# Performance work log

Measured on AMD Instinct MI355X. Metric: run time of the kernel, lower is better.

## Reference

```python
import jax, jax.numpy as jnp
import numpy as np

B, OBS, LAT, NXT, E, HG, H = 8192, 128, 32, 128, 8, 256, 256


def setup_inputs() -> dict:
    key = jax.random.key(0)
    ks = jax.random.split(key, 20)
    d_in = OBS + LAT

    def w(k, shape, fan_in):
        return jax.random.uniform(k, shape, jnp.float32, -1.0, 1.0) * (np.sqrt(3.0) / np.sqrt(fan_in)).astype(np.float32)

    inp = {
        "x": jax.random.normal(ks[0], (B, OBS), jnp.float32),
        "z": jax.random.normal(ks[1], (B, LAT), jnp.float32),
        # gating MLP: (obs+lat) -> hg -> hg -> hg -> E
        "gw0": w(ks[2], (d_in, HG), d_in), "gb0": jnp.zeros((HG,), jnp.float32),
        "gw1": w(ks[3], (HG, HG), HG),    "gb1": jnp.zeros((HG,), jnp.float32),
        "gw2": w(ks[4], (HG, HG), HG),    "gb2": jnp.zeros((HG,), jnp.float32),
        "gw3": w(ks[5], (HG, E), HG),     "gb3": jnp.zeros((E,), jnp.float32),
        # expert weight stacks (kaiming-uniform-style init, bias = 0.01)
        "w0": w(ks[6], (E, d_in, H), d_in * H),      "b0": jnp.full((E, H), 0.01, jnp.float32),
        "w1": w(ks[7], (E, H + LAT, H), (H + LAT) * H), "b1": jnp.full((E, H), 0.01, jnp.float32),
        "w2": w(ks[8], (E, H + LAT, NXT), (H + LAT) * NXT), "b2": jnp.full((E, NXT), 0.01, jnp.float32),
    }
    return inp


def reference(x, z, gw0, gb0, gw1, gb1, gw2, gb2, gw3, gb3, w0, b0, w1, b1, w2, b2):
    xz = jnp.concatenate((x, z), axis=1)  # [B, obs+lat]
    # gating MLP (ELU activations, linear head) -> softmax coefficients over experts
    g = jax.nn.elu(xz @ gw0 + gb0)
    g = jax.nn.elu(g @ gw1 + gb1)
    g = jax.nn.elu(g @ gw2 + gb2)
    coef = jax.nn.softmax(g @ gw3 + gb3, axis=1)  # [B, E]

    layer_out = x
    for w, b, act in ((w0, b0, jax.nn.elu), (w1, b1, jax.nn.elu), (w2, b2, None)):
        inp = jnp.concatenate((layer_out, z), axis=1)  # [B, i]
        # coefficient-weighted expert mixing fused with the per-sample matvec:
        # equals (coef @ flat_weight).view(B,i,o) consumed by baddbmm in the original
        out = jnp.einsum('bi,eio,be->bo', inp, w, coef) + coef @ b
        layer_out = act(out) if act is not None else out
    return layer_out
```

## Files before the change

### kernel.cpp

```cpp
#include <hip/hip_runtime.h>
#include <hip/hip_bf16.h>

typedef _Float16 half_t;
typedef __attribute__((ext_vector_type(8))) _Float16 half8;
typedef __attribute__((ext_vector_type(4))) _Float16 half4;
typedef __attribute__((ext_vector_type(4))) float float4v;
typedef __attribute__((ext_vector_type(2))) float float2v;

#define BSZ 8192
#define NT 1024
#define ACTSTR 280
#define XSTR 152
#define ZSTR 40

#define OFF_SX 0
#define OFF_SB0 (OFF_SX + 32 * XSTR)
#define OFF_SB1 (OFF_SB0 + 32 * ACTSTR)
#define OFF_SZ (OFF_SB1 + 32 * ACTSTR)
#define HALFS_TOTAL (OFF_SZ + 32 * ZSTR)
#define OFF_LOG_B (HALFS_TOTAL * 2)
#define OFF_CF_B (OFF_LOG_B + 1024)
#define SMEM_BYTES 131072

__device__ __forceinline__ float elu_fast(float v) {
    return v > 0.f ? v : (__expf(v) - 1.f);
}

template <int EXPP, int NPASS, int CH, int MT, bool ZLAST, int ACT, int DST>
__device__ __forceinline__ void layer_run(
    const half_t* sSrc, int sstr, const half_t* sZ,
    const half_t* __restrict__ W, int NS,
    const float* __restrict__ bias, int biasN, const float* sCf,
    half_t* sDst, float* __restrict__ gOut, int ldg,
    int row0, int strip, int mrow, int lane, int l15, int quad) {
    constexpr int TOT = NPASS * CH;
    const size_t estr = (size_t)NS * CH * 512;
    const int col = strip * 16 + l15;
    const half_t* aBase = sSrc + (mrow + l15) * sstr + quad * 8;
    const half_t* zBase = sZ + (mrow + l15) * ZSTR + quad * 8;

    const half_t* wp = W + (size_t)strip * CH * 512 + lane * 8;
    int c_i = 0;
    const float* bp = bias + col;
    int c_c = 0, h_c = 0;

    half8 B0[EXPP], B1[EXPP], A0[MT], A1[MT];
    float part[MT][4];
    float bv[EXPP];
    float4v acc[EXPP][MT];

    auto issue = [&](half8(&B)[EXPP], half8(&A)[MT]) {
#pragma unroll
        for (int e = 0; e < EXPP; ++e) B[e] = *(const half8*)&wp[(size_t)e * estr];
#pragma unroll
        for (int mt = 0; mt < MT; ++mt)
            A[mt] = (ZLAST && c_i == CH - 1)
                        ? *(const half8*)&zBase[mt * 16 * ZSTR]
                        : *(const half8*)&aBase[mt * 16 * sstr + c_i * 32];
        wp += 512;
        if (++c_i == CH) { c_i = 0; wp += (size_t)EXPP * estr - (size_t)CH * 512; }
    };

    auto body = [&](half8(&B)[EXPP], half8(&A)[MT]) {
        if (c_c == 0) {
#pragma unroll
            for (int e = 0; e < EXPP; ++e) bv[e] = bp[(size_t)e * biasN];
#pragma unroll
            for (int e = 0; e < EXPP; ++e)
#pragma unroll
                for (int mt = 0; mt < MT; ++mt) acc[e][mt] = (float4v){0.f, 0.f, 0.f, 0.f};
        }
#pragma unroll
        for (int e = 0; e < EXPP; ++e)
#pragma unroll
            for (int mt = 0; mt < MT; ++mt)
                acc[e][mt] = __builtin_amdgcn_mfma_f32_16x16x32_f16(A[mt], B[e], acc[e][mt], 0, 0, 0);
        if (c_c == CH - 1) {
#pragma unroll
            for (int mt = 0; mt < MT; ++mt)
#pragma unroll
                for (int r = 0; r < 4; ++r) {
                    const int rl = mrow + mt * 16 + quad * 4 + r;
                    float val;
                    if constexpr (EXPP * NPASS == 1) {
                        val = acc[0][mt][r] + bv[0];
                    } else {
                        const float2v cf = *(const float2v*)&sCf[rl * 8 + h_c * EXPP];
                        val = cf[0] * (acc[0][mt][r] + bv[0]);
                        val += cf[1] * (acc[1][mt][r] + bv[1]);
                    }
                    part[mt][r] = (h_c == 0) ? val : part[mt][r] + val;
                    if (h_c == NPASS - 1) {
                        float o = part[mt][r];
                        if (DST == 0) {
                            if (ACT) o = elu_fast(o);
                            sDst[rl * ACTSTR + col] = (half_t)o;
                        } else {
                            gOut[(size_t)(row0 + rl) * ldg + col] = o;
                        }
                    }
                }
            bp += (size_t)EXPP * biasN;
        }
        if (++c_c == CH) { c_c = 0; ++h_c; }
    };

    issue(B0, A0);
    int it = 0;
#pragma unroll 1
    for (; it + 2 < TOT; it += 2) {
        issue(B1, A1);
        body(B0, A0);
        issue(B0, A0);
        body(B1, A1);
    }
    if constexpr (TOT % 2 == 0) {
        issue(B1, A1);
        body(B0, A0);
        body(B1, A1);
    } else {
        body(B0, A0);
    }
}

__device__ __forceinline__ void layer_logits(
    const half_t* sSrc, const half_t* __restrict__ W,
    const float* __restrict__ bias, float* sLog, int wv, int lane, int l15, int quad) {
    if (wv != 0) return;
    float4v acc[2] = {(float4v){0.f, 0.f, 0.f, 0.f}, (float4v){0.f, 0.f, 0.f, 0.f}};
#pragma unroll
    for (int c = 0; c < 8; ++c) {
        half8 a0 = *(const half8*)&sSrc[l15 * ACTSTR + c * 32 + quad * 8];
        half8 a1 = *(const half8*)&sSrc[(16 + l15) * ACTSTR + c * 32 + quad * 8];
        half8 b = *(const half8*)&W[c * 512 + lane * 8];
        acc[0] = __builtin_amdgcn_mfma_f32_16x16x32_f16(a0, b, acc[0], 0, 0, 0);
        acc[1] = __builtin_amdgcn_mfma_f32_16x16x32_f16(a1, b, acc[1], 0, 0, 0);
    }
    if (l15 < 8) {
        const float bvv = bias[l15];
#pragma unroll
        for (int mt = 0; mt < 2; ++mt)
#pragma unroll
            for (int r = 0; r < 4; ++r)
                sLog[(mt * 16 + quad * 4 + r) * 8 + l15] = acc[mt][r] + bvv;
    }
}

__global__ __launch_bounds__(NT) void fused_mann(
    const float* __restrict__ x, const float* __restrict__ z,
    const half_t* __restrict__ Wg0, const half_t* __restrict__ Wg1,
    const half_t* __restrict__ Wg2, const half_t* __restrict__ Wg3,
    const float* __restrict__ gb0, const float* __restrict__ gb1,
    const float* __restrict__ gb2, const float* __restrict__ gb3,
    const half_t* __restrict__ W0, const half_t* __restrict__ W1,
    const half_t* __restrict__ W2, const float* __restrict__ b0,
    const float* __restrict__ b1, const float* __restrict__ b2,
    float* __restrict__ out) {
    extern __shared__ __align__(16) char dynsm[];
    half_t* sm = (half_t*)dynsm;
    half_t* sX = sm + OFF_SX;
    half_t* sB0 = sm + OFF_SB0;
    half_t* sB1 = sm + OFF_SB1;
    half_t* sZ = sm + OFF_SZ;
    float* sLog = (float*)(dynsm + OFF_LOG_B);
    float* sCf = (float*)(dynsm + OFF_CF_B);

    const int tid = threadIdx.x;
    const int row0 = blockIdx.x * 32;
    const int lane = tid & 63, wv = tid >> 6;
    const int l15 = lane & 15, quad = lane >> 4;

    for (int i = tid; i < 32 * 128; i += NT) {
        int r = i >> 7, c = i & 127;
        sX[r * XSTR + c] = (half_t)x[(size_t)(row0 + r) * 128 + c];
    }
    for (int i = tid; i < 32 * 32; i += NT) {
        int r = i >> 5, c = i & 31;
        sZ[r * ZSTR + c] = (half_t)z[(size_t)(row0 + r) * 32 + c];
    }
    __syncthreads();

    layer_run<1, 1, 5, 2, true, 1, 0>(sX, XSTR, sZ, Wg0, 16, gb0, 256, nullptr,
                                      sB0, nullptr, 0, row0, wv, 0, lane, l15, quad);
    __syncthreads();
    layer_run<1, 1, 8, 2, false, 1, 0>(sB0, ACTSTR, sZ, Wg1, 16, gb1, 256, nullptr,
                                       sB1, nullptr, 0, row0, wv, 0, lane, l15, quad);
    __syncthreads();
    layer_run<1, 1, 8, 2, false, 1, 0>(sB1, ACTSTR, sZ, Wg2, 16, gb2, 256, nullptr,
                                       sB0, nullptr, 0, row0, wv, 0, lane, l15, quad);
    __syncthreads();
    layer_logits(sB0, Wg3, gb3, sLog, wv, lane, l15, quad);
    __syncthreads();
    if (tid < 32) {
        float v[8], m = -1e30f;
#pragma unroll
        for (int e = 0; e < 8; ++e) { v[e] = sLog[tid * 8 + e]; m = fmaxf(m, v[e]); }
        float sum = 0.f;
#pragma unroll
        for (int e = 0; e < 8; ++e) { v[e] = __expf(v[e] - m); sum += v[e]; }
        float inv = 1.f / sum;
#pragma unroll
        for (int e = 0; e < 8; ++e) sCf[tid * 8 + e] = v[e] * inv;
    }
    __syncthreads();
    layer_run<2, 4, 5, 2, true, 1, 0>(sX, XSTR, sZ, W0, 16, b0, 256, sCf,
                                      sB1, nullptr, 0, row0, wv, 0, lane, l15, quad);
    __syncthreads();
    layer_run<2, 4, 9, 2, true, 1, 0>(sB1, ACTSTR, sZ, W1, 16, b1, 256, sCf,
                                      sB0, nullptr, 0, row0, wv, 0, lane, l15, quad);
    __syncthreads();
    layer_run<2, 4, 9, 1, true, 0, 2>(sB0, ACTSTR, sZ, W2, 8, b2, 128, sCf,
                                      nullptr, out, 128, row0, wv & 7, (wv >> 3) * 16,
                                      lane, l15, quad);
}

struct WDesc { const float* src; half_t* dst; int K, N, Npad, blk0; };
struct WPack { WDesc d[7]; };

__global__ __launch_bounds__(256) void conv_w_all(WPack pk) {
    __shared__ float t[32][33];
    const int bid = blockIdx.x;
    int di = 0;
#pragma unroll
    for (int i = 1; i < 7; ++i)
        if (bid >= pk.d[i].blk0) di = i;
    const WDesc d = pk.d[di];
    const int NS = d.Npad >> 4, CHN = d.K >> 5;
    const int ntiles = d.Npad / 32, ktiles = CHN;
    int local = bid - d.blk0;
    const int e = local / (ktiles * ntiles);
    local %= ktiles * ntiles;
    const int k0 = (local / ntiles) * 32, n0 = (local % ntiles) * 32;
    const int tr = threadIdx.x >> 3;
    const int tc = (threadIdx.x & 7) * 4;

    float4 v = {0.f, 0.f, 0.f, 0.f};
    if (n0 + tc < d.N)
        v = *(const float4*)&d.src[((size_t)e * d.K + k0 + tr) * d.N + n0 + tc];
    t[tr][tc] = v.x; t[tr][tc + 1] = v.y; t[tr][tc + 2] = v.z; t[tr][tc + 3] = v.w;
    __syncthreads();
    half4 h;
#pragma unroll
    for (int i = 0; i < 4; ++i) h[i] = (half_t)t[tc + i][tr];
    const int n = n0 + tr;
    const size_t blk = ((size_t)e * NS + (n >> 4)) * CHN + (k0 >> 5);
    const int off = ((tc >> 3) * 16 + (n & 15)) * 8 + (tc & 7);
    *(half4*)&d.dst[blk * 512 + off] = h;
}

extern "C" void kernel_launch(void* const* d_in, const int* in_sizes, int n_in,
                              void* d_out, int out_size, void* d_ws, size_t ws_size,
                              hipStream_t stream) {
    const float* x   = (const float*)d_in[0];
    const float* z   = (const float*)d_in[1];
    const float* gw0 = (const float*)d_in[2];
    const float* gb0 = (const float*)d_in[3];
    const float* gw1 = (const float*)d_in[4];
    const float* gb1 = (const float*)d_in[5];
    const float* gw2 = (const float*)d_in[6];
    const float* gb2 = (const float*)d_in[7];
    const float* gw3 = (const float*)d_in[8];
    const float* gb3 = (const float*)d_in[9];
    const float* w0  = (const float*)d_in[10];
    const float* b0  = (const float*)d_in[11];
    const float* w1  = (const float*)d_in[12];
    const float* b1  = (const float*)d_in[13];
    const float* w2  = (const float*)d_in[14];
    const float* b2  = (const float*)d_in[15];

    char* p = (char*)d_ws;
    auto take = [&](size_t bytes) { char* r = p; p += bytes; return r; };
    half_t* Wg0 = (half_t*)take((size_t)256 * 160 * 2);
    half_t* Wg1 = (half_t*)take((size_t)256 * 256 * 2);
    half_t* Wg2 = (half_t*)take((size_t)256 * 256 * 2);
    half_t* Wg3 = (half_t*)take((size_t)32 * 256 * 2);
    half_t* W0  = (half_t*)take((size_t)8 * 256 * 160 * 2);
    half_t* W1  = (half_t*)take((size_t)8 * 256 * 288 * 2);
    half_t* W2  = (half_t*)take((size_t)8 * 128 * 288 * 2);
    float* out  = (float*)d_out;

    WPack pk;
    int blk = 0;
    auto mk = [&](int i, const float* s, half_t* dst, int K, int N, int Npad, int E) {
        pk.d[i] = WDesc{s, dst, K, N, Npad, blk};
        blk += E * (K / 32) * (Npad / 32);
    };
    mk(0, gw0, Wg0, 160, 256, 256, 1);
    mk(1, gw1, Wg1, 256, 256, 256, 1);
    mk(2, gw2, Wg2, 256, 256, 256, 1);
    mk(3, gw3, Wg3, 256, 8, 32, 1);
    mk(4, w0, W0, 160, 256, 256, 8);
    mk(5, w1, W1, 288, 256, 256, 8);
    mk(6, w2, W2, 288, 128, 128, 8);

    hipFuncSetAttribute((const void*)fused_mann,
                        hipFuncAttributeMaxDynamicSharedMemorySize, SMEM_BYTES);

    conv_w_all<<<dim3(blk), dim3(256), 0, stream>>>(pk);
    fused_mann<<<dim3(BSZ / 32), dim3(NT), SMEM_BYTES, stream>>>(
        x, z, Wg0, Wg1, Wg2, Wg3, gb0, gb1, gb2, gb3,
        W0, W1, W2, b0, b1, b2, out);
}
```

Measured before the change: 131.3 us.

## Stream one expert's weights through per-wave LDS ring via global_load_lds DMA

In the expert-mixing layers, one of the two expert weight streams is now loaded with direct global-to-LDS DMA into a per-wave 3-slot ring. The other stream stays in registers, and explicit vmcnt waits pipeline the two. Expert biases are preloaded into shared memory per wave. The aim is to cut VGPR pressure and overlap weight fetch with MFMA work, at the cost of extra LDS traffic, more shared memory, and hand-tuned waitcnt ordering that is fragile.

```diff
diff --git a/kernel.cpp b/kernel.cpp
--- a/kernel.cpp
+++ b/kernel.cpp
@@ -13,113 +13,214 @@
 #define XSTR 152
 #define ZSTR 40
 
-#define OFF_SX 0
+#define RING_WAVE 1536
+#define OFF_SX (16 * RING_WAVE)
 #define OFF_SB0 (OFF_SX + 32 * XSTR)
 #define OFF_SB1 (OFF_SB0 + 32 * ACTSTR)
 #define OFF_SZ (OFF_SB1 + 32 * ACTSTR)
 #define HALFS_TOTAL (OFF_SZ + 32 * ZSTR)
-#define OFF_LOG_B (HALFS_TOTAL * 2)
+#define OFF_BIAS_B (HALFS_TOTAL * 2)
+#define OFF_LOG_B (OFF_BIAS_B + 8192)
 #define OFF_CF_B (OFF_LOG_B + 1024)
-#define SMEM_BYTES 131072
+#define SMEM_BYTES (OFF_CF_B + 1024)
 
 __device__ __forceinline__ float elu_fast(float v) {
     return v > 0.f ? v : (__expf(v) - 1.f);
 }
 
+template <int N>
+__device__ __forceinline__ void wait_vm() {
+    if constexpr (N == 0)      asm volatile("s_waitcnt vmcnt(0)" ::: "memory");
+    else if constexpr (N == 1) asm volatile("s_waitcnt vmcnt(1)" ::: "memory");
+    else if constexpr (N == 2) asm volatile("s_waitcnt vmcnt(2)" ::: "memory");
+    else if constexpr (N == 3) asm volatile("s_waitcnt vmcnt(3)" ::: "memory");
+    else                       asm volatile("s_waitcnt vmcnt(4)" ::: "memory");
+}
+
+__device__ __forceinline__ void lds_dma16(half_t* lds, const half_t* g) {
+    __builtin_amdgcn_global_load_lds(
+        (const __attribute__((address_space(1))) void*)g,
+        (__attribute__((address_space(3))) void*)lds, 16, 0, 0);
+}
+
 template <int EXPP, int NPASS, int CH, int MT, bool ZLAST, int ACT, int DST>
 __device__ __forceinline__ void layer_run(
-    const half_t* sSrc, int sstr, const half_t* sZ,
+    half_t* sm, const half_t* sSrc, int sstr, const half_t* sZ,
     const half_t* __restrict__ W, int NS,
-    const float* __restrict__ bias, int biasN, const float* sCf,
+    const float* __restrict__ bias, int biasN, const float* sCf, float* sBias,
     half_t* sDst, float* __restrict__ gOut, int ldg,
-    int row0, int strip, int mrow, int lane, int l15, int quad) {
+    int row0, int strip, int mrow, int wv, int lane, int l15, int quad) {
     constexpr int TOT = NPASS * CH;
+    constexpr bool DMA = (EXPP == 2);
     const size_t estr = (size_t)NS * CH * 512;
     const int col = strip * 16 + l15;
     const half_t* aBase = sSrc + (mrow + l15) * sstr + quad * 8;
     const half_t* zBase = sZ + (mrow + l15) * ZSTR + quad * 8;
 
-    const half_t* wp = W + (size_t)strip * CH * 512 + lane * 8;
-    int c_i = 0;
-    const float* bp = bias + col;
+    float part[MT][4];
+    float4v acc[EXPP][MT];
     int c_c = 0, h_c = 0;
 
-    half8 B0[EXPP], B1[EXPP], A0[MT], A1[MT];
-    float part[MT][4];
-    float bv[EXPP];
-    float4v acc[EXPP][MT];
-
-    auto issue = [&](half8(&B)[EXPP], half8(&A)[MT]) {
-#pragma unroll
-        for (int e = 0; e < EXPP; ++e) B[e] = *(const half8*)&wp[(size_t)e * estr];
-#pragma unroll
-        for (int mt = 0; mt < MT; ++mt)
-            A[mt] = (ZLAST && c_i == CH - 1)
-                        ? *(const half8*)&zBase[mt * 16 * ZSTR]
-                        : *(const half8*)&aBase[mt * 16 * sstr + c_i * 32];
-        wp += 512;
-        if (++c_i == CH) { c_i = 0; wp += (size_t)EXPP * estr - (size_t)CH * 512; }
-    };
-
-    auto body = [&](half8(&B)[EXPP], half8(&A)[MT]) {
-        if (c_c == 0) {
-#pragma unroll
-            for (int e = 0; e < EXPP; ++e) bv[e] = bp[(size_t)e * biasN];
+    if constexpr (!DMA) {
+        const half_t* wp = W + (size_t)strip * CH * 512 + lane * 8;
+        int c_i = 0;
+        const float* bp = bias + col;
+        half8 B0[EXPP], B1[EXPP], A0[MT], A1[MT];
+        float bv[EXPP];
+
+        auto issue = [&](half8(&B)[EXPP], half8(&A)[MT]) {
+#pragma unroll
+            for (int e = 0; e < EXPP; ++e) B[e] = *(const half8*)&wp[(size_t)e * estr];
+#pragma unroll
+            for (int mt = 0; mt < MT; ++mt)
+                A[mt] = (ZLAST && c_i == CH - 1)
+                            ? *(const half8*)&zBase[mt * 16 * ZSTR]
+                            : *(const half8*)&aBase[mt * 16 * sstr + c_i * 32];
+            wp += 512;
+            if (++c_i == CH) { c_i = 0; wp += (size_t)EXPP * estr - (size_t)CH * 512; }
+        };
+        auto body = [&](half8(&B)[EXPP], half8(&A)[MT]) {
+            if (c_c == 0) {
+#pragma unroll
+                for (int e = 0; e < EXPP; ++e) bv[e] = bp[(size_t)e * biasN];
+#pragma unroll
+                for (int e = 0; e < EXPP; ++e)
+#pragma unroll
+                    for (int mt = 0; mt < MT; ++mt) acc[e][mt] = (float4v){0.f, 0.f, 0.f, 0.f};
+            }
 #pragma unroll
             for (int e = 0; e < EXPP; ++e)
 #pragma unroll
-                for (int mt = 0; mt < MT; ++mt) acc[e][mt] = (float4v){0.f, 0.f, 0.f, 0.f};
-        }
-#pragma unroll
-        for (int e = 0; e < EXPP; ++e)
-#pragma unroll
-            for (int mt = 0; mt < MT; ++mt)
-                acc[e][mt] = __builtin_amdgcn_mfma_f32_16x16x32_f16(A[mt], B[e], acc[e][mt], 0, 0, 0);
-        if (c_c == CH - 1) {
-#pragma unroll
-            for (int mt = 0; mt < MT; ++mt)
-#pragma unroll
-                for (int r = 0; r < 4; ++r) {
-                    const int rl = mrow + mt * 16 + quad * 4 + r;
-                    float val;
-                    if constexpr (EXPP * NPASS == 1) {
-                        val = acc[0][mt][r] + bv[0];
-                    } else {
-                        const float2v cf = *(const float2v*)&sCf[rl * 8 + h_c * EXPP];
-                        val = cf[0] * (acc[0][mt][r] + bv[0]);
-                        val += cf[1] * (acc[1][mt][r] + bv[1]);
-                    }
-                    part[mt][r] = (h_c == 0) ? val : part[mt][r] + val;
-                    if (h_c == NPASS - 1) {
-                        float o = part[mt][r];
-                        if (DST == 0) {
+                for (int mt = 0; mt < MT; ++mt)
+                    acc[e][mt] = __builtin_amdgcn_mfma_f32_16x16x32_f16(A[mt], B[e], acc[e][mt], 0, 0, 0);
+            if (c_c == CH - 1) {
+#pragma unroll
+                for (int mt = 0; mt < MT; ++mt)
+#pragma unroll
+                    for (int r = 0; r < 4; ++r) {
+                        const int rl = mrow + mt * 16 + quad * 4 + r;
+                        float val = acc[0][mt][r] + bv[0];
+                        part[mt][r] = (h_c == 0) ? val : part[mt][r] + val;
+                        if (h_c == NPASS - 1) {
+                            float o = part[mt][r];
                             if (ACT) o = elu_fast(o);
                             sDst[rl * ACTSTR + col] = (half_t)o;
-                        } else {
-                            gOut[(size_t)(row0 + rl) * ldg + col] = o;
                         }
                     }
-                }
-            bp += (size_t)EXPP * biasN;
+            }
+            if (++c_c == CH) { c_c = 0; ++h_c; }
+        };
+
+        issue(B0, A0);
+        int it = 0;
+#pragma unroll 1
+        for (; it + 2 < TOT; it += 2) {
+            issue(B1, A1);
+            body(B0, A0);
+            issue(B0, A0);
+            body(B1, A1);
         }
-        if (++c_c == CH) { c_c = 0; ++h_c; }
-    };
-
-    issue(B0, A0);
-    int it = 0;
+        if constexpr (TOT % 2 == 0) {
+            issue(B1, A1);
+            body(B0, A0);
+            body(B1, A1);
+        } else {
+            body(B0, A0);
+        }
+    } else {
+        static_assert(TOT % 2 == 0, "hybrid drain assumes even TOT");
+        half_t* myring = sm + wv * RING_WAVE;
+        float* myBias = sBias + wv * 128;
+        if (quad == 0) {
+#pragma unroll
+            for (int e = 0; e < NPASS * 2; ++e)
+                myBias[e * 16 + l15] = bias[(size_t)e * biasN + col];
+        }
+        wait_vm<0>();
+
+        const half_t* wp0 = W + (size_t)strip * CH * 512 + lane * 8;
+        const half_t* wp1 = W + (size_t)strip * CH * 512 + lane * 8 + estr;
+        int c0 = 0, c1 = 0, s_i = 0, s_c = 0;
+
+        auto dma = [&]() {
+            lds_dma16(myring + s_i * 512, wp0);
+            s_i = (s_i == 2) ? 0 : s_i + 1;
+            wp0 += 512;
+            if (++c0 == CH) { c0 = 0; wp0 += (size_t)2 * estr - (size_t)CH * 512; }
+        };
+        half8 R0, R1, A0[MT], A1[MT];
+        auto rissue = [&](half8& R, half8(&A)[MT]) {
+            R = *(const half8*)wp1;
+#pragma unroll
+            for (int mt = 0; mt < MT; ++mt)
+                A[mt] = (ZLAST && c1 == CH - 1)
+                            ? *(const half8*)&zBase[mt * 16 * ZSTR]
+                            : *(const half8*)&aBase[mt * 16 * sstr + c1 * 32];
+            wp1 += 512;
+            if (++c1 == CH) { c1 = 0; wp1 += (size_t)2 * estr - (size_t)CH * 512; }
+        };
+        auto body = [&](half8& R, half8(&A)[MT]) {
+            if (c_c == 0) {
+#pragma unroll
+                for (int e = 0; e < 2; ++e)
+#pragma unroll
+                    for (int mt = 0; mt < MT; ++mt) acc[e][mt] = (float4v){0.f, 0.f, 0.f, 0.f};
+            }
+            const half_t* sp = myring + s_c * 512 + lane * 8;
+            half8 b0 = *(const half8*)sp;
+#pragma unroll
+            for (int mt = 0; mt < MT; ++mt)
+                acc[0][mt] = __builtin_amdgcn_mfma_f32_16x16x32_f16(A[mt], b0, acc[0][mt], 0, 0, 0);
+#pragma unroll
+            for (int mt = 0; mt < MT; ++mt)
+                acc[1][mt] = __builtin_amdgcn_mfma_f32_16x16x32_f16(A[mt], R, acc[1][mt], 0, 0, 0);
+            if (c_c == CH - 1) {
+                const float bv0 = myBias[(h_c * 2 + 0) * 16 + l15];
+                const float bv1 = myBias[(h_c * 2 + 1) * 16 + l15];
+#pragma unroll
+                for (int mt = 0; mt < MT; ++mt)
+#pragma unroll
+                    for (int r = 0; r < 4; ++r) {
+                        const int rl = mrow + mt * 16 + quad * 4 + r;
+                        const float2v cf = *(const float2v*)&sCf[rl * 8 + h_c * 2];
+                        float val = cf[0] * (acc[0][mt][r] + bv0);
+                        val += cf[1] * (acc[1][mt][r] + bv1);
+                        part[mt][r] = (h_c == 0) ? val : part[mt][r] + val;
+                        if (h_c == NPASS - 1) {
+                            float o = part[mt][r];
+                            if (DST == 0) {
+                                if (ACT) o = elu_fast(o);
+                                sDst[rl * ACTSTR + col] = (half_t)o;
+                            } else {
+                                gOut[(size_t)(row0 + rl) * ldg + col] = o;
+                            }
+                        }
+                    }
+            }
+            s_c = (s_c == 2) ? 0 : s_c + 1;
+            if (++c_c == CH) { c_c = 0; ++h_c; }
+        };
+
+        dma();
+        dma();
+        rissue(R0, A0);
+        int it = 0;
 #pragma unroll 1
-    for (; it + 2 < TOT; it += 2) {
-        issue(B1, A1);
-        body(B0, A0);
-        issue(B0, A0);
-        body(B1, A1);
-    }
-    if constexpr (TOT % 2 == 0) {
-        issue(B1, A1);
-        body(B0, A0);
-        body(B1, A1);
-    } else {
-        body(B0, A0);
+        for (; it + 2 < TOT; it += 2) {
+            dma();
+            rissue(R1, A1);
+            wait_vm<4>();
+            body(R0, A0);
+            dma();
+            rissue(R0, A0);
+            wait_vm<4>();
+            body(R1, A1);
+        }
+        rissue(R1, A1);
+        wait_vm<3>();
+        body(R0, A0);
+        wait_vm<1>();
+        body(R1, A1);
     }
 }
 
@@ -162,6 +263,7 @@
     half_t* sB0 = sm + OFF_SB0;
     half_t* sB1 = sm + OFF_SB1;
     half_t* sZ = sm + OFF_SZ;
+    float* sBias = (float*)(dynsm + OFF_BIAS_B);
     float* sLog = (float*)(dynsm + OFF_LOG_B);
     float* sCf = (float*)(dynsm + OFF_CF_B);
 
@@ -180,14 +282,14 @@
     }
     __syncthreads();
 
-    layer_run<1, 1, 5, 2, true, 1, 0>(sX, XSTR, sZ, Wg0, 16, gb0, 256, nullptr,
-                                      sB0, nullptr, 0, row0, wv, 0, lane, l15, quad);
-    __syncthreads();
-    layer_run<1, 1, 8, 2, false, 1, 0>(sB0, ACTSTR, sZ, Wg1, 16, gb1, 256, nullptr,
-                                       sB1, nullptr, 0, row0, wv, 0, lane, l15, quad);
-    __syncthreads();
-    layer_run<1, 1, 8, 2, false, 1, 0>(sB1, ACTSTR, sZ, Wg2, 16, gb2, 256, nullptr,
-                                       sB0, nullptr, 0, row0, wv, 0, lane, l15, quad);
+    layer_run<1, 1, 5, 2, true, 1, 0>(sm, sX, XSTR, sZ, Wg0, 16, gb0, 256, nullptr, sBias,
+                                      sB0, nullptr, 0, row0, wv, 0, wv, lane, l15, quad);
+    __syncthreads();
+    layer_run<1, 1, 8, 2, false, 1, 0>(sm, sB0, ACTSTR, sZ, Wg1, 16, gb1, 256, nullptr, sBias,
+                                       sB1, nullptr, 0, row0, wv, 0, wv, lane, l15, quad);
+    __syncthreads();
+    layer_run<1, 1, 8, 2, false, 1, 0>(sm, sB1, ACTSTR, sZ, Wg2, 16, gb2, 256, nullptr, sBias,
+                                       sB0, nullptr, 0, row0, wv, 0, wv, lane, l15, quad);
     __syncthreads();
     layer_logits(sB0, Wg3, gb3, sLog, wv, lane, l15, quad);
     __syncthreads();
@@ -203,15 +305,15 @@
         for (int e = 0; e < 8; ++e) sCf[tid * 8 + e] = v[e] * inv;
     }
     __syncthreads();
-    layer_run<2, 4, 5, 2, true, 1, 0>(sX, XSTR, sZ, W0, 16, b0, 256, sCf,
-                                      sB1, nullptr, 0, row0, wv, 0, lane, l15, quad);
-    __syncthreads();
-    layer_run<2, 4, 9, 2, true, 1, 0>(sB1, ACTSTR, sZ, W1, 16, b1, 256, sCf,
-                                      sB0, nullptr, 0, row0, wv, 0, lane, l15, quad);
-    __syncthreads();
-    layer_run<2, 4, 9, 1, true, 0, 2>(sB0, ACTSTR, sZ, W2, 8, b2, 128, sCf,
+    layer_run<2, 4, 5, 2, true, 1, 0>(sm, sX, XSTR, sZ, W0, 16, b0, 256, sCf, sBias,
+                                      sB1, nullptr, 0, row0, wv, 0, wv, lane, l15, quad);
+    __syncthreads();
+    layer_run<2, 4, 9, 2, true, 1, 0>(sm, sB1, ACTSTR, sZ, W1, 16, b1, 256, sCf, sBias,
+                                      sB0, nullptr, 0, row0, wv, 0, wv, lane, l15, quad);
+    __syncthreads();
+    layer_run<2, 4, 9, 1, true, 0, 2>(sm, sB0, ACTSTR, sZ, W2, 8, b2, 128, sCf, sBias,
                                       nullptr, out, 128, row0, wv & 7, (wv >> 3) * 16,
-                                      lane, l15, quad);
+                                      wv, lane, l15, quad);
 }
 
 struct WDesc { const float* src; half_t* dst; int K, N, Npad, blk0; };
```

Result: slower. 138.2 us (+5.3%).
